# Kernel tuning notes

Measured on AMD Instinct MI355X. Metric: run time of the kernel, lower is better.

Reference implementation:

```python
import jax, jax.numpy as jnp
import numpy as np

N_ENTITY = 100000
N_RELATION = 32
DIM = 64
N_LAYER = 2
B = 4096
T = 64


def setup_inputs() -> dict:
    key = jax.random.key(0)
    ks = jax.random.split(key, 12)
    inp = {
        "items": jax.random.randint(ks[0], (B,), 0, N_ENTITY),
        "user_h": jax.random.randint(ks[1], (N_LAYER, B, T), 0, N_ENTITY),
        "user_r": jax.random.randint(ks[2], (N_LAYER, B, T), 0, N_RELATION),
        "user_t": jax.random.randint(ks[3], (N_LAYER, B, T), 0, N_ENTITY),
        "item_h": jax.random.randint(ks[4], (N_LAYER, B, T), 0, N_ENTITY),
        "item_r": jax.random.randint(ks[5], (N_LAYER, B, T), 0, N_RELATION),
        "item_t": jax.random.randint(ks[6], (N_LAYER, B, T), 0, N_ENTITY),
        # parameters (xavier-ish scale)
        "entity_emb": jax.random.normal(ks[7], (N_ENTITY, DIM), jnp.float32) * 0.05,
        "relation_emb": jax.random.normal(ks[8], (N_RELATION, DIM), jnp.float32) * 0.05,
        # torch Linear(in,out,bias=False) stored here as [in, out] so y = x @ W
        "W1": jax.random.normal(ks[9], (2 * DIM, DIM), jnp.float32) * 0.1,
        "W2": jax.random.normal(ks[10], (DIM, DIM), jnp.float32) * 0.1,
        "W3": jax.random.normal(ks[11], (DIM, 1), jnp.float32) * 0.1,
    }
    return inp


def reference(items, user_h, user_r, user_t, item_h, item_r, item_t,
              entity_emb, relation_emb, W1, W2, W3):
    def knowledge_attention(h_idx, r_idx, t_idx):
        h = entity_emb[h_idx]        # [B, T, d]
        r = relation_emb[r_idx]      # [B, T, d]
        t = entity_emb[t_idx]        # [B, T, d]
        x = jnp.concatenate([h, r], axis=-1)           # [B, T, 2d]
        a = jax.nn.relu(x @ W1)                        # [B, T, d]
        a = jax.nn.relu(a @ W2)                        # [B, T, d]
        a = jax.nn.sigmoid(jnp.squeeze(a @ W3, -1))    # [B, T]
        w = jax.nn.softmax(a, axis=-1)                 # softmax over triples
        return jnp.sum(w[..., None] * t, axis=1)       # [B, d]

    # user embeddings: origin = mean of hop-0 heads, then attention per layer; agg='sum'
    e_u = jnp.mean(entity_emb[user_h[0]], axis=1)
    for i in range(N_LAYER):
        e_u = e_u + knowledge_attention(user_h[i], user_r[i], user_t[i])

    # item embeddings: origin = item entity emb, attention per layer,
    # plus (agg=='sum', n_layer>0) extra mean of hop-0 heads
    e_v = entity_emb[items]
    for i in range(N_LAYER):
        e_v = e_v + knowledge_attention(item_h[i], item_r[i], item_t[i])
    e_v = e_v + jnp.mean(entity_emb[item_h[0]], axis=1)

    scores = jax.nn.sigmoid(jnp.sum(e_v * e_u, axis=1))  # [B]
    return scores
```

## Files before the change

### kernel.cpp

```cpp
#include <hip/hip_runtime.h>
#include <hip/hip_bf16.h>
#include <cstdint>

#define DEV static __device__ __forceinline__

typedef float        v4f __attribute__((ext_vector_type(4)));
typedef float        v2f __attribute__((ext_vector_type(2)));
typedef short        v8s __attribute__((ext_vector_type(8)));
typedef unsigned int v4u __attribute__((ext_vector_type(4)));

static constexpr int N_ENT = 100000;
static constexpr int BATCH = 4096;

DEV unsigned short f2bf(float f) {
    __hip_bfloat16 h = __float2bfloat16(f);
    return __builtin_bit_cast(unsigned short, h);
}
DEV unsigned int pkbf(float lo, float hi) {
    return (unsigned)f2bf(lo) | ((unsigned)f2bf(hi) << 16);
}
DEV float bflo(unsigned int w) { return __uint_as_float(w << 16); }
DEV float bfhi(unsigned int w) { return __uint_as_float(w & 0xffff0000u); }
DEV v2f up2(unsigned int w) { return (v2f){bflo(w), bfhi(w)}; }

__global__ void k0_prep(const float* __restrict__ rel, const float* __restrict__ W1,
                        const float* __restrict__ W2,
                        unsigned short* __restrict__ R1b, unsigned short* __restrict__ W2p,
                        unsigned short* __restrict__ W1p)
{
    const int gid = blockIdx.x * 256 + threadIdx.x;
    if (gid < 2048) {
        const int r = gid >> 6, j = gid & 63;
        float acc = 0.f;
        #pragma unroll 8
        for (int k = 0; k < 64; ++k)
            acc += rel[r * 64 + k] * W1[(64 + k) * 64 + j];
        R1b[gid] = f2bf(acc);
    } else if (gid < 2048 + 4096) {
        const int f = gid - 2048;
        const int i = f & 7, l = (f >> 3) & 63;
        const int tn = (f >> 9) & 3, kk = f >> 11;
        W2p[f] = f2bf(W2[(32 * kk + 8 * (l >> 4) + i) * 64 + 16 * tn + (l & 15)]);
    } else if (gid < 2048 + 8192) {
        const int f = gid - 6144;
        const int i = f & 7, l = (f >> 3) & 63;
        const int tn = (f >> 9) & 3, kk = f >> 11;
        W1p[f] = f2bf(W1[(32 * kk + 8 * (l >> 4) + i) * 64 + 16 * tn + (l & 15)]);
    }
}

__global__ void __launch_bounds__(256) k1_e1(const float* __restrict__ emb,
                                             const unsigned short* __restrict__ W1p,
                                             unsigned short* __restrict__ E1,
                                             unsigned short* __restrict__ E0)
{
    const int lane = threadIdx.x & 63;
    const int q = lane & 15, g = lane >> 4;
    const int wid = blockIdx.x * 4 + (threadIdx.x >> 6);
    const int e0 = wid * 16;
    if (e0 >= N_ENT) return;

    v8s af[2];
    #pragma unroll
    for (int kk = 0; kk < 2; ++kk) {
        const float* p = emb + (size_t)(e0 + q) * 64 + 32 * kk + 8 * g;
        const v4f x = *(const v4f*)p;
        const v4f y = *(const v4f*)(p + 4);
        v4u pk;
        pk[0] = pkbf(x[0], x[1]); pk[1] = pkbf(x[2], x[3]);
        pk[2] = pkbf(y[0], y[1]); pk[3] = pkbf(y[2], y[3]);
        af[kk] = __builtin_bit_cast(v8s, pk);
        *(v4u*)(E0 + (size_t)(e0 + q) * 64 + 32 * kk + 8 * g) = pk;
    }

    v4f acc[4];
    #pragma unroll
    for (int tn = 0; tn < 4; ++tn) acc[tn] = (v4f){0.f, 0.f, 0.f, 0.f};
    #pragma unroll
    for (int kk = 0; kk < 2; ++kk)
        #pragma unroll
        for (int tn = 0; tn < 4; ++tn) {
            const v8s bfr = *(const v8s*)(W1p + ((kk * 4 + tn) * 64 + lane) * 8);
            acc[tn] = __builtin_amdgcn_mfma_f32_16x16x32_bf16(af[kk], bfr, acc[tn], 0, 0, 0);
        }
    #pragma unroll
    for (int tn = 0; tn < 4; ++tn)
        #pragma unroll
        for (int i = 0; i < 4; ++i)
            E1[(size_t)(e0 + 4 * g + i) * 64 + 16 * tn + q] = f2bf(acc[tn][i]);
}

__global__ void __launch_bounds__(256) k2_fused(
    const int* __restrict__ items,
    const int* __restrict__ user_h, const int* __restrict__ user_r, const int* __restrict__ user_t,
    const int* __restrict__ item_h, const int* __restrict__ item_r, const int* __restrict__ item_t,
    const float* __restrict__ emb, const unsigned short* __restrict__ E0,
    const unsigned short* __restrict__ E1,
    const unsigned short* __restrict__ R1b, const unsigned short* __restrict__ W2p,
    const float* __restrict__ W3, float* __restrict__ out)
{
    __shared__ float ws_w[4][64];
    __shared__ float att_s[4][64];
    __shared__ float mp[4][64];

    const int lane  = threadIdx.x & 63;
    const int b     = blockIdx.x;
    const int combo = threadIdx.x >> 6;
    const int layer = combo & 1;
    const int side  = combo >> 1, half = combo & 1;
    const int* Hp; const int* Rp; const int* Tp;
    if (combo < 2) { Hp = user_h; Rp = user_r; Tp = user_t; }
    else           { Hp = item_h; Rp = item_r; Tp = item_t; }
    const int base = (layer * BATCH + b) * 64;
    const int* H0p = (side ? item_h : user_h) + b * 64;

    const int q = lane & 15, g = lane >> 4;
    const int sub = lane & 7, grp = lane >> 3;

    int hidx[4], ridx[4];
    #pragma unroll
    for (int tm = 0; tm < 4; ++tm) {
        hidx[tm] = Hp[base + 16 * tm + q];
        ridx[tm] = Rp[base + 16 * tm + q];
    }
    const int tv = Tp[base + lane];
    int midx[4];
    #pragma unroll
    for (int it = 0; it < 4; ++it) midx[it] = H0p[32 * half + 8 * it + grp];

    v4u ev[4][2], rv[4][2];
    #pragma unroll
    for (int tm = 0; tm < 4; ++tm)
        #pragma unroll
        for (int kk = 0; kk < 2; ++kk) {
            ev[tm][kk] = *(const v4u*)(E1  + (size_t)hidx[tm] * 64 + 32 * kk + 8 * g);
            rv[tm][kk] = *(const v4u*)(R1b + (size_t)ridx[tm] * 64 + 32 * kk + 8 * g);
        }
    v4u e0v[8];
    #pragma unroll
    for (int it = 0; it < 8; ++it) {
        const int tr = __shfl(tv, 8 * it + grp);
        e0v[it] = *(const v4u*)(E0 + (size_t)tr * 64 + sub * 8);
    }
    v4u m0v[4];
    #pragma unroll
    for (int it = 0; it < 4; ++it)
        m0v[it] = *(const v4u*)(E0 + (size_t)midx[it] * 64 + sub * 8);
    float itemv = (combo == 0) ? emb[(size_t)items[b] * 64 + lane] : 0.f;

    #pragma unroll
    for (int it = 0; it < 8; ++it) asm volatile("" : "+v"(e0v[it]));
    #pragma unroll
    for (int it = 0; it < 4; ++it) asm volatile("" : "+v"(m0v[it]));
    asm volatile("" : "+v"(itemv));

    float w3v[4];
    #pragma unroll
    for (int tn = 0; tn < 4; ++tn) w3v[tn] = W3[16 * tn + q];

    float p[4][4];
    #pragma unroll
    for (int tm = 0; tm < 4; ++tm) {
        v4f a4[4];
        #pragma unroll
        for (int tn = 0; tn < 4; ++tn) a4[tn] = (v4f){0.f, 0.f, 0.f, 0.f};
        #pragma unroll
        for (int kk = 0; kk < 2; ++kk) {
            v4u afu;
            #pragma unroll
            for (int w = 0; w < 4; ++w) {
                const unsigned int e = ev[tm][kk][w], r = rv[tm][kk][w];
                afu[w] = pkbf(fmaxf(bflo(e) + bflo(r), 0.f),
                              fmaxf(bfhi(e) + bfhi(r), 0.f));
            }
            const v8s af = __builtin_bit_cast(v8s, afu);
            #pragma unroll
            for (int tn = 0; tn < 4; ++tn) {
                const v8s bfr = *(const v8s*)(W2p + ((kk * 4 + tn) * 64 + lane) * 8);
                a4[tn] = __builtin_amdgcn_mfma_f32_16x16x32_bf16(af, bfr, a4[tn], 0, 0, 0);
            }
        }
        #pragma unroll
        for (int i = 0; i < 4; ++i) {
            float s = 0.f;
            #pragma unroll
            for (int tn = 0; tn < 4; ++tn)
                s += fmaxf(a4[tn][i], 0.f) * w3v[tn];
            p[tm][i] = s;
        }
    }
    #pragma unroll
    for (int m = 1; m <= 8; m <<= 1)
        #pragma unroll
        for (int tm = 0; tm < 4; ++tm)
            #pragma unroll
            for (int i = 0; i < 4; ++i)
                p[tm][i] += __shfl_xor(p[tm][i], m);

    float ee[4][4];
    float sloc = 0.f;
    #pragma unroll
    for (int tm = 0; tm < 4; ++tm)
        #pragma unroll
        for (int i = 0; i < 4; ++i) {
            const float sg = 1.f / (1.f + __expf(-p[tm][i]));
            const float ex = __expf(sg);
            ee[tm][i] = ex;
            sloc += ex;
        }
    sloc += __shfl_xor(sloc, 16);
    sloc += __shfl_xor(sloc, 32);
    const float rS = 1.f / sloc;

    if (q == 0) {
        #pragma unroll
        for (int tm = 0; tm < 4; ++tm) {
            v4f wv;
            #pragma unroll
            for (int i = 0; i < 4; ++i) wv[i] = ee[tm][i] * rS;
            *(v4f*)&ws_w[combo][16 * tm + 4 * g] = wv;
        }
    }

    v2f a2[4], m2[4];
    #pragma unroll
    for (int c = 0; c < 4; ++c) { a2[c] = (v2f){0.f, 0.f}; m2[c] = (v2f){0.f, 0.f}; }
    #pragma unroll
    for (int it = 0; it < 8; ++it) {
        const float w = ws_w[combo][8 * it + grp];
        const v2f wv = (v2f){w, w};
        const v4u e = e0v[it];
        #pragma unroll
        for (int c = 0; c < 4; ++c) a2[c] += wv * up2(e[c]);
    }
    #pragma unroll
    for (int it = 0; it < 4; ++it) {
        const v4u e = m0v[it];
        #pragma unroll
        for (int c = 0; c < 4; ++c) m2[c] += up2(e[c]);
    }
    #pragma unroll
    for (int m = 8; m <= 32; m <<= 1)
        #pragma unroll
        for (int c = 0; c < 4; ++c) {
            a2[c][0] += __shfl_xor(a2[c][0], m);
            a2[c][1] += __shfl_xor(a2[c][1], m);
            m2[c][0] += __shfl_xor(m2[c][0], m);
            m2[c][1] += __shfl_xor(m2[c][1], m);
        }
    if (lane < 8) {
        #pragma unroll
        for (int c = 0; c < 4; ++c) {
            att_s[combo][lane * 8 + 2 * c]     = a2[c][0];
            att_s[combo][lane * 8 + 2 * c + 1] = a2[c][1];
            mp[combo][lane * 8 + 2 * c]        = m2[c][0];
            mp[combo][lane * 8 + 2 * c + 1]    = m2[c][1];
        }
    }
    __syncthreads();

    if (threadIdx.x < 64) {
        const int j = lane;
        const float eu = att_s[0][j] + att_s[1][j] + (mp[0][j] + mp[1][j]) * (1.f / 64.f);
        const float evv = itemv + att_s[2][j] + att_s[3][j]
                        + (mp[2][j] + mp[3][j]) * (1.f / 64.f);
        float d = eu * evv;
        #pragma unroll
        for (int m = 1; m <= 32; m <<= 1) d += __shfl_xor(d, m);
        if (lane == 0) out[b] = 1.f / (1.f + __expf(-d));
    }
}

extern "C" void kernel_launch(void* const* d_in, const int* in_sizes, int n_in,
                              void* d_out, int out_size, void* d_ws, size_t ws_size,
                              hipStream_t stream)
{
    const int*   items  = (const int*)d_in[0];
    const int*   user_h = (const int*)d_in[1];
    const int*   user_r = (const int*)d_in[2];
    const int*   user_t = (const int*)d_in[3];
    const int*   item_h = (const int*)d_in[4];
    const int*   item_r = (const int*)d_in[5];
    const int*   item_t = (const int*)d_in[6];
    const float* emb    = (const float*)d_in[7];
    const float* rel    = (const float*)d_in[8];
    const float* W1     = (const float*)d_in[9];
    const float* W2     = (const float*)d_in[10];
    const float* W3     = (const float*)d_in[11];
    float* out = (float*)d_out;

    char* ws = (char*)d_ws;
    const size_t tb = (size_t)N_ENT * 64 * 2;
    unsigned short* E0  = (unsigned short*)ws;
    unsigned short* E1  = (unsigned short*)(ws + tb);
    unsigned short* R1b = (unsigned short*)(ws + 2 * tb);
    unsigned short* W2p = (unsigned short*)(ws + 2 * tb + 4096);
    unsigned short* W1p = (unsigned short*)(ws + 2 * tb + 4096 + 8192);

    hipLaunchKernelGGL(k0_prep, dim3(40), dim3(256), 0, stream, rel, W1, W2, R1b, W2p, W1p);
    hipLaunchKernelGGL(k1_e1, dim3((6250 + 3) / 4), dim3(256), 0, stream, emb, W1p, E1, E0);
    hipLaunchKernelGGL(k2_fused, dim3(BATCH), dim3(256), 0, stream,
                       items, user_h, user_r, user_t, item_h, item_r, item_t,
                       emb, E0, E1, R1b, W2p, W3, out);
}
```

Measured before the change: 94.51 us.

## Switch attention intermediates to fp16 and process two batch rows per block

The precomputed E1 and R1 tables and W2 now use fp16, so the add and ReLU run as packed half-precision vector ops feeding f16 MFMA instead of per-element bf16 unpack and repack. k1 swaps MFMA operands so each lane writes contiguous 64-bit chunks of E1. k2 processes two batch elements per 512-thread block, hoists the W2 fragment loads out of the tile loop, drops the asm register barriers and uses fast exp2 and rcp intrinsics. The changes aim to cut conversion ALU work and launch overhead, at the cost of fp16 range and precision limits and higher register pressure.

```diff
diff --git a/kernel.cpp b/kernel.cpp
--- a/kernel.cpp
+++ b/kernel.cpp
@@ -8,6 +8,7 @@
 typedef float        v2f __attribute__((ext_vector_type(2)));
 typedef short        v8s __attribute__((ext_vector_type(8)));
 typedef unsigned int v4u __attribute__((ext_vector_type(4)));
+typedef _Float16     v8h __attribute__((ext_vector_type(8)));
 
 static constexpr int N_ENT = 100000;
 static constexpr int BATCH = 4096;
@@ -22,27 +23,36 @@
 DEV float bflo(unsigned int w) { return __uint_as_float(w << 16); }
 DEV float bfhi(unsigned int w) { return __uint_as_float(w & 0xffff0000u); }
 DEV v2f up2(unsigned int w) { return (v2f){bflo(w), bfhi(w)}; }
+DEV unsigned int pkh(float a, float b) {
+    return __builtin_bit_cast(unsigned int, __builtin_amdgcn_cvt_pkrtz(a, b));
+}
+DEV float fexp(float x) { return __builtin_amdgcn_exp2f(1.44269504f * x); }
+DEV float frcp(float x) { return __builtin_amdgcn_rcpf(x); }
 
 __global__ void k0_prep(const float* __restrict__ rel, const float* __restrict__ W1,
                         const float* __restrict__ W2,
-                        unsigned short* __restrict__ R1b, unsigned short* __restrict__ W2p,
+                        unsigned short* __restrict__ R1h, unsigned short* __restrict__ W2ph,
                         unsigned short* __restrict__ W1p)
 {
     const int gid = blockIdx.x * 256 + threadIdx.x;
-    if (gid < 2048) {
-        const int r = gid >> 6, j = gid & 63;
-        float acc = 0.f;
+    if (gid < 1024) {
+        const int r = gid >> 5, jp = gid & 31;
+        float d0 = 0.f, d1 = 0.f;
         #pragma unroll 8
-        for (int k = 0; k < 64; ++k)
-            acc += rel[r * 64 + k] * W1[(64 + k) * 64 + j];
-        R1b[gid] = f2bf(acc);
-    } else if (gid < 2048 + 4096) {
-        const int f = gid - 2048;
+        for (int k = 0; k < 64; ++k) {
+            const float rv = rel[r * 64 + k];
+            d0 += rv * W1[(64 + k) * 64 + 2 * jp];
+            d1 += rv * W1[(64 + k) * 64 + 2 * jp + 1];
+        }
+        ((unsigned int*)R1h)[r * 32 + jp] = pkh(d0, d1);
+    } else if (gid < 1024 + 4096) {
+        const int f = gid - 1024;
         const int i = f & 7, l = (f >> 3) & 63;
         const int tn = (f >> 9) & 3, kk = f >> 11;
-        W2p[f] = f2bf(W2[(32 * kk + 8 * (l >> 4) + i) * 64 + 16 * tn + (l & 15)]);
-    } else if (gid < 2048 + 8192) {
-        const int f = gid - 6144;
+        const _Float16 hv = (_Float16)W2[(32 * kk + 8 * (l >> 4) + i) * 64 + 16 * tn + (l & 15)];
+        W2ph[f] = __builtin_bit_cast(unsigned short, hv);
+    } else if (gid < 1024 + 8192) {
+        const int f = gid - 5120;
         const int i = f & 7, l = (f >> 3) & 63;
         const int tn = (f >> 9) & 3, kk = f >> 11;
         W1p[f] = f2bf(W1[(32 * kk + 8 * (l >> 4) + i) * 64 + 16 * tn + (l & 15)]);
@@ -51,7 +61,7 @@
 
 __global__ void __launch_bounds__(256) k1_e1(const float* __restrict__ emb,
                                              const unsigned short* __restrict__ W1p,
-                                             unsigned short* __restrict__ E1,
+                                             unsigned short* __restrict__ E1h,
                                              unsigned short* __restrict__ E0)
 {
     const int lane = threadIdx.x & 63;
@@ -60,7 +70,7 @@
     const int e0 = wid * 16;
     if (e0 >= N_ENT) return;
 
-    v8s af[2];
+    v8s bf[2];
     #pragma unroll
     for (int kk = 0; kk < 2; ++kk) {
         const float* p = emb + (size_t)(e0 + q) * 64 + 32 * kk + 8 * g;
@@ -69,45 +79,50 @@
         v4u pk;
         pk[0] = pkbf(x[0], x[1]); pk[1] = pkbf(x[2], x[3]);
         pk[2] = pkbf(y[0], y[1]); pk[3] = pkbf(y[2], y[3]);
-        af[kk] = __builtin_bit_cast(v8s, pk);
+        bf[kk] = __builtin_bit_cast(v8s, pk);
         *(v4u*)(E0 + (size_t)(e0 + q) * 64 + 32 * kk + 8 * g) = pk;
     }
 
     v4f acc[4];
     #pragma unroll
-    for (int tn = 0; tn < 4; ++tn) acc[tn] = (v4f){0.f, 0.f, 0.f, 0.f};
+    for (int tile = 0; tile < 4; ++tile) acc[tile] = (v4f){0.f, 0.f, 0.f, 0.f};
     #pragma unroll
     for (int kk = 0; kk < 2; ++kk)
         #pragma unroll
-        for (int tn = 0; tn < 4; ++tn) {
-            const v8s bfr = *(const v8s*)(W1p + ((kk * 4 + tn) * 64 + lane) * 8);
-            acc[tn] = __builtin_amdgcn_mfma_f32_16x16x32_bf16(af[kk], bfr, acc[tn], 0, 0, 0);
-        }
-    #pragma unroll
-    for (int tn = 0; tn < 4; ++tn)
-        #pragma unroll
-        for (int i = 0; i < 4; ++i)
-            E1[(size_t)(e0 + 4 * g + i) * 64 + 16 * tn + q] = f2bf(acc[tn][i]);
-}
-
-__global__ void __launch_bounds__(256) k2_fused(
+        for (int tile = 0; tile < 4; ++tile) {
+            const v8s w1f = *(const v8s*)(W1p + ((kk * 4 + tile) * 64 + lane) * 8);
+            acc[tile] = __builtin_amdgcn_mfma_f32_16x16x32_bf16(w1f, bf[kk], acc[tile], 0, 0, 0);
+        }
+    #pragma unroll
+    for (int tile = 0; tile < 4; ++tile) {
+        unsigned int u[2];
+        u[0] = pkh(acc[tile][0], acc[tile][1]);
+        u[1] = pkh(acc[tile][2], acc[tile][3]);
+        *(unsigned long long*)(E1h + (size_t)(e0 + q) * 64 + 16 * tile + 4 * g) =
+            ((unsigned long long)u[1] << 32) | u[0];
+    }
+}
+
+__global__ void __launch_bounds__(512) k2_fused(
     const int* __restrict__ items,
     const int* __restrict__ user_h, const int* __restrict__ user_r, const int* __restrict__ user_t,
     const int* __restrict__ item_h, const int* __restrict__ item_r, const int* __restrict__ item_t,
     const float* __restrict__ emb, const unsigned short* __restrict__ E0,
-    const unsigned short* __restrict__ E1,
-    const unsigned short* __restrict__ R1b, const unsigned short* __restrict__ W2p,
+    const unsigned short* __restrict__ E1h,
+    const unsigned short* __restrict__ R1h, const unsigned short* __restrict__ W2ph,
     const float* __restrict__ W3, float* __restrict__ out)
 {
-    __shared__ float ws_w[4][64];
-    __shared__ float att_s[4][64];
-    __shared__ float mp[4][64];
+    __shared__ float ws_w[8][64];
+    __shared__ float att_s[8][64];
+    __shared__ float mp[8][64];
 
     const int lane  = threadIdx.x & 63;
-    const int b     = blockIdx.x;
-    const int combo = threadIdx.x >> 6;
+    const int w     = threadIdx.x >> 6;
+    const int elem  = w >> 2;
+    const int combo = w & 3;
     const int layer = combo & 1;
     const int side  = combo >> 1, half = combo & 1;
+    const int b     = blockIdx.x * 2 + elem;
     const int* Hp; const int* Rp; const int* Tp;
     if (combo < 2) { Hp = user_h; Rp = user_r; Tp = user_t; }
     else           { Hp = item_h; Rp = item_r; Tp = item_t; }
@@ -133,8 +148,8 @@
     for (int tm = 0; tm < 4; ++tm)
         #pragma unroll
         for (int kk = 0; kk < 2; ++kk) {
-            ev[tm][kk] = *(const v4u*)(E1  + (size_t)hidx[tm] * 64 + 32 * kk + 8 * g);
-            rv[tm][kk] = *(const v4u*)(R1b + (size_t)ridx[tm] * 64 + 32 * kk + 8 * g);
+            ev[tm][kk] = *(const v4u*)(E1h + (size_t)hidx[tm] * 64 + 32 * kk + 8 * g);
+            rv[tm][kk] = *(const v4u*)(R1h + (size_t)ridx[tm] * 64 + 32 * kk + 8 * g);
         }
     v4u e0v[8];
     #pragma unroll
@@ -146,19 +161,19 @@
     #pragma unroll
     for (int it = 0; it < 4; ++it)
         m0v[it] = *(const v4u*)(E0 + (size_t)midx[it] * 64 + sub * 8);
-    float itemv = (combo == 0) ? emb[(size_t)items[b] * 64 + lane] : 0.f;
-
-    #pragma unroll
-    for (int it = 0; it < 8; ++it) asm volatile("" : "+v"(e0v[it]));
-    #pragma unroll
-    for (int it = 0; it < 4; ++it) asm volatile("" : "+v"(m0v[it]));
-    asm volatile("" : "+v"(itemv));
 
     float w3v[4];
     #pragma unroll
     for (int tn = 0; tn < 4; ++tn) w3v[tn] = W3[16 * tn + q];
+    v8h bfr[2][4];
+    #pragma unroll
+    for (int kk = 0; kk < 2; ++kk)
+        #pragma unroll
+        for (int tn = 0; tn < 4; ++tn)
+            bfr[kk][tn] = __builtin_bit_cast(v8h, *(const v4u*)(W2ph + ((kk * 4 + tn) * 64 + lane) * 8));
 
     float p[4][4];
+    const v8h zz = {};
     #pragma unroll
     for (int tm = 0; tm < 4; ++tm) {
         v4f a4[4];
@@ -166,19 +181,12 @@
         for (int tn = 0; tn < 4; ++tn) a4[tn] = (v4f){0.f, 0.f, 0.f, 0.f};
         #pragma unroll
         for (int kk = 0; kk < 2; ++kk) {
-            v4u afu;
+            const v8h e = __builtin_bit_cast(v8h, ev[tm][kk]);
+            const v8h r = __builtin_bit_cast(v8h, rv[tm][kk]);
+            const v8h af = __builtin_elementwise_max(e + r, zz);
             #pragma unroll
-            for (int w = 0; w < 4; ++w) {
-                const unsigned int e = ev[tm][kk][w], r = rv[tm][kk][w];
-                afu[w] = pkbf(fmaxf(bflo(e) + bflo(r), 0.f),
-                              fmaxf(bfhi(e) + bfhi(r), 0.f));
-            }
-            const v8s af = __builtin_bit_cast(v8s, afu);
-            #pragma unroll
-            for (int tn = 0; tn < 4; ++tn) {
-                const v8s bfr = *(const v8s*)(W2p + ((kk * 4 + tn) * 64 + lane) * 8);
-                a4[tn] = __builtin_amdgcn_mfma_f32_16x16x32_bf16(af, bfr, a4[tn], 0, 0, 0);
-            }
+            for (int tn = 0; tn < 4; ++tn)
+                a4[tn] = __builtin_amdgcn_mfma_f32_16x16x32_f16(af, bfr[kk][tn], a4[tn], 0, 0, 0);
         }
         #pragma unroll
         for (int i = 0; i < 4; ++i) {
@@ -203,14 +211,14 @@
     for (int tm = 0; tm < 4; ++tm)
         #pragma unroll
         for (int i = 0; i < 4; ++i) {
-            const float sg = 1.f / (1.f + __expf(-p[tm][i]));
-            const float ex = __expf(sg);
+            const float sg = frcp(1.f + fexp(-p[tm][i]));
+            const float ex = fexp(sg);
             ee[tm][i] = ex;
             sloc += ex;
         }
     sloc += __shfl_xor(sloc, 16);
     sloc += __shfl_xor(sloc, 32);
-    const float rS = 1.f / sloc;
+    const float rS = frcp(sloc);
 
     if (q == 0) {
         #pragma unroll
@@ -218,7 +226,7 @@
             v4f wv;
             #pragma unroll
             for (int i = 0; i < 4; ++i) wv[i] = ee[tm][i] * rS;
-            *(v4f*)&ws_w[combo][16 * tm + 4 * g] = wv;
+            *(v4f*)&ws_w[w][16 * tm + 4 * g] = wv;
         }
     }
 
@@ -227,8 +235,8 @@
     for (int c = 0; c < 4; ++c) { a2[c] = (v2f){0.f, 0.f}; m2[c] = (v2f){0.f, 0.f}; }
     #pragma unroll
     for (int it = 0; it < 8; ++it) {
-        const float w = ws_w[combo][8 * it + grp];
-        const v2f wv = (v2f){w, w};
+        const float wg = ws_w[w][8 * it + grp];
+        const v2f wv = (v2f){wg, wg};
         const v4u e = e0v[it];
         #pragma unroll
         for (int c = 0; c < 4; ++c) a2[c] += wv * up2(e[c]);
@@ -251,23 +259,26 @@
     if (lane < 8) {
         #pragma unroll
         for (int c = 0; c < 4; ++c) {
-            att_s[combo][lane * 8 + 2 * c]     = a2[c][0];
-            att_s[combo][lane * 8 + 2 * c + 1] = a2[c][1];
-            mp[combo][lane * 8 + 2 * c]        = m2[c][0];
-            mp[combo][lane * 8 + 2 * c + 1]    = m2[c][1];
+            att_s[w][lane * 8 + 2 * c]     = a2[c][0];
+            att_s[w][lane * 8 + 2 * c + 1] = a2[c][1];
+            mp[w][lane * 8 + 2 * c]        = m2[c][0];
+            mp[w][lane * 8 + 2 * c + 1]    = m2[c][1];
         }
     }
     __syncthreads();
 
-    if (threadIdx.x < 64) {
+    if (combo == 0) {
         const int j = lane;
-        const float eu = att_s[0][j] + att_s[1][j] + (mp[0][j] + mp[1][j]) * (1.f / 64.f);
-        const float evv = itemv + att_s[2][j] + att_s[3][j]
-                        + (mp[2][j] + mp[3][j]) * (1.f / 64.f);
+        const int e4 = elem * 4;
+        const float itemv = emb[(size_t)items[b] * 64 + j];
+        const float eu = att_s[e4 + 0][j] + att_s[e4 + 1][j]
+                       + (mp[e4 + 0][j] + mp[e4 + 1][j]) * (1.f / 64.f);
+        const float evv = itemv + att_s[e4 + 2][j] + att_s[e4 + 3][j]
+                       + (mp[e4 + 2][j] + mp[e4 + 3][j]) * (1.f / 64.f);
         float d = eu * evv;
         #pragma unroll
         for (int m = 1; m <= 32; m <<= 1) d += __shfl_xor(d, m);
-        if (lane == 0) out[b] = 1.f / (1.f + __expf(-d));
+        if (lane == 0) out[b] = frcp(1.f + fexp(-d));
     }
 }
 
@@ -291,15 +302,15 @@
 
     char* ws = (char*)d_ws;
     const size_t tb = (size_t)N_ENT * 64 * 2;
-    unsigned short* E0  = (unsigned short*)ws;
-    unsigned short* E1  = (unsigned short*)(ws + tb);
-    unsigned short* R1b = (unsigned short*)(ws + 2 * tb);
-    unsigned short* W2p = (unsigned short*)(ws + 2 * tb + 4096);
-    unsigned short* W1p = (unsigned short*)(ws + 2 * tb + 4096 + 8192);
-
-    hipLaunchKernelGGL(k0_prep, dim3(40), dim3(256), 0, stream, rel, W1, W2, R1b, W2p, W1p);
-    hipLaunchKernelGGL(k1_e1, dim3((6250 + 3) / 4), dim3(256), 0, stream, emb, W1p, E1, E0);
-    hipLaunchKernelGGL(k2_fused, dim3(BATCH), dim3(256), 0, stream,
+    unsigned short* E0   = (unsigned short*)ws;
+    unsigned short* E1h  = (unsigned short*)(ws + tb);
+    unsigned short* R1h  = (unsigned short*)(ws + 2 * tb);
+    unsigned short* W2ph = (unsigned short*)(ws + 2 * tb + 4096);
+    unsigned short* W1p  = (unsigned short*)(ws + 2 * tb + 4096 + 8192);
+
+    hipLaunchKernelGGL(k0_prep, dim3(36), dim3(256), 0, stream, rel, W1, W2, R1h, W2ph, W1p);
+    hipLaunchKernelGGL(k1_e1, dim3((6250 + 3) / 4), dim3(256), 0, stream, emb, W1p, E1h, E0);
+    hipLaunchKernelGGL(k2_fused, dim3(BATCH / 2), dim3(512), 0, stream,
                        items, user_h, user_r, user_t, item_h, item_r, item_t,
-                       emb, E0, E1, R1b, W2p, W3, out);
-}
+                       emb, E0, E1h, R1h, W2ph, W3, out);
+}
```

Measured after the change: 100.0 us. +5.8%, slower.
